# Performance work log

Measured on AMD Instinct MI355X. Metric: run time of the kernel, lower is better.

## Reference

```python
import jax, jax.numpy as jnp
import numpy as np

B, N, IN_CH = 16, 2048, 128
H, C = 4, 64
HC = H * C
E = 524288
NT = B * N
FC0, FC1 = 1024, 512
OMIC = 128
OUT = 2
LN_EPS = 1e-5


def setup_inputs() -> dict:
    key = jax.random.key(0)
    ks = jax.random.split(key, 32)
    s = 0.02
    d = {}
    d['x'] = jax.random.normal(ks[0], (NT, IN_CH), jnp.float32)
    d['edge_index'] = jax.random.randint(ks[1], (2, E), 0, NT, dtype=jnp.int64)
    # GATConv 1: Linear(IN_CH, H*C, bias=False), att_src/att_dst [H,C], bias [H*C]
    d['w1'] = jax.random.normal(ks[2], (IN_CH, HC), jnp.float32) * s
    d['att_src1'] = jax.random.normal(ks[3], (H, C), jnp.float32) * s
    d['att_dst1'] = jax.random.normal(ks[4], (H, C), jnp.float32) * s
    d['bias1'] = jnp.zeros((HC,), jnp.float32)
    d['pool1_w'] = jax.random.normal(ks[5], (HC, 1), jnp.float32) * s
    d['pool1_b'] = jnp.zeros((1,), jnp.float32)
    # GATConv 2: in = H*C
    d['w2'] = jax.random.normal(ks[6], (HC, HC), jnp.float32) * s
    d['att_src2'] = jax.random.normal(ks[7], (H, C), jnp.float32) * s
    d['att_dst2'] = jax.random.normal(ks[8], (H, C), jnp.float32) * s
    d['bias2'] = jnp.zeros((HC,), jnp.float32)
    d['pool2_w'] = jax.random.normal(ks[9], (HC, 1), jnp.float32) * s
    d['pool2_b'] = jnp.zeros((1,), jnp.float32)
    # LayerNorm(num_nodes)
    d['ln_w'] = jnp.ones((N,), jnp.float32)
    d['ln_b'] = jnp.zeros((N,), jnp.float32)
    # FC encoder: Linear(3N, FC0)+ELU, Linear(FC0, FC1)+ELU, Linear(FC1, OMIC)+ELU
    d['enc0_w'] = jax.random.normal(ks[10], (3 * N, FC0), jnp.float32) * s
    d['enc0_b'] = jnp.zeros((FC0,), jnp.float32)
    d['enc1_w'] = jax.random.normal(ks[11], (FC0, FC1), jnp.float32) * s
    d['enc1_b'] = jnp.zeros((FC1,), jnp.float32)
    d['enc2_w'] = jax.random.normal(ks[12], (FC1, OMIC), jnp.float32) * s
    d['enc2_b'] = jnp.zeros((OMIC,), jnp.float32)
    d['last_w'] = jax.random.normal(ks[13], (OMIC, OUT), jnp.float32) * s
    d['last_b'] = jnp.zeros((OUT,), jnp.float32)
    return d


def layer_norm(v, w, b):
    mu = jnp.mean(v, axis=-1, keepdims=True)
    var = jnp.mean((v - mu) ** 2, axis=-1, keepdims=True)
    return (v - mu) * jax.lax.rsqrt(var + LN_EPS) * w + b


def gat_conv(x, src, dst, w, att_src, att_dst, bias):
    # x: [NT, F_in] -> transformed per head [NT, H, C]
    xw = (x @ w).reshape(NT, H, C)
    a_src = jnp.einsum('nhc,hc->nh', xw, att_src)  # [NT, H]
    a_dst = jnp.einsum('nhc,hc->nh', xw, att_dst)
    alpha = jax.nn.leaky_relu(a_src[src] + a_dst[dst], negative_slope=0.2)  # [E', H]
    amax = jax.ops.segment_max(alpha, dst, num_segments=NT)
    ea = jnp.exp(alpha - amax[dst])
    denom = jax.ops.segment_sum(ea, dst, num_segments=NT)
    coef = ea / (denom[dst] + 1e-16)
    msg = xw[src] * coef[:, :, None]  # [E', H, C]
    out = jax.ops.segment_sum(msg, dst, num_segments=NT)
    return out.reshape(NT, HC) + bias


def reference(x, edge_index, w1, att_src1, att_dst1, bias1, pool1_w, pool1_b,
              w2, att_src2, att_dst2, bias2, pool2_w, pool2_b,
              ln_w, ln_b, enc0_w, enc0_b, enc1_w, enc1_b, enc2_w, enc2_b,
              last_w, last_b):
    # add self-loops (GATConv default)
    loops = jnp.arange(NT, dtype=edge_index.dtype)
    src = jnp.concatenate([edge_index[0], loops])
    dst = jnp.concatenate([edge_index[1], loops])
    # layer1 feature: per-node mean, densified to [B, N]
    x0 = layer_norm(jnp.mean(x, axis=-1).reshape(B, N), ln_w, ln_b)
    # GAT layer 1 (dropout is identity in eval)
    h = jax.nn.elu(gat_conv(x, src, dst, w1, att_src1, att_dst1, bias1))
    x1 = layer_norm((h @ pool1_w + pool1_b)[:, 0].reshape(B, N), ln_w, ln_b)
    # GAT layer 2
    h = jax.nn.elu(gat_conv(h, src, dst, w2, att_src2, att_dst2, bias2))
    x2 = layer_norm((h @ pool2_w + pool2_b)[:, 0].reshape(B, N), ln_w, ln_b)
    feat = jnp.concatenate([x0, x1, x2], axis=1)  # [B, 3N]
    e = jax.nn.elu(feat @ enc0_w + enc0_b)
    e = jax.nn.elu(e @ enc1_w + enc1_b)
    e = jax.nn.elu(e @ enc2_w + enc2_b)
    return e @ last_w + last_b  # [B, OUT]
```

## Files before the change

kernel.cpp:

```cpp
#include <hip/hip_runtime.h>
#include <math.h>

#define NTN 32768
#define BB 16
#define NN 2048
#define IN_CH 128
#define HC 256
#define EREAL 524288
#define ETOT (EREAL + NTN)
#define FC0 1024
#define FC1 512
#define OMIC 128
#define OUTD 2
#define CAP 96

#define PREP_BLKS (NTN / 4)
#define DEG_BLKS (EREAL / 256)
#define CASTW_BLKS ((HC * IN_CH + HC * HC) / 256)

typedef __attribute__((ext_vector_type(8))) short bf16x8;
typedef __attribute__((ext_vector_type(4))) float f32x4;

static __device__ __forceinline__ float wave_sum(float v) {
    for (int o = 32; o; o >>= 1) v += __shfl_xor(v, o);
    return v;
}
static __device__ __forceinline__ unsigned short f2bf(float f) {
    unsigned u = __float_as_uint(f);
    unsigned r = (u + 0x7fff + ((u >> 16) & 1)) >> 16;
    return (unsigned short)r;
}
static __device__ __forceinline__ void fma8(uint4 v, float e, float* acc) {
    acc[0] += __uint_as_float(v.x << 16) * e;
    acc[1] += __uint_as_float(v.x & 0xffff0000u) * e;
    acc[2] += __uint_as_float(v.y << 16) * e;
    acc[3] += __uint_as_float(v.y & 0xffff0000u) * e;
    acc[4] += __uint_as_float(v.z << 16) * e;
    acc[5] += __uint_as_float(v.z & 0xffff0000u) * e;
    acc[6] += __uint_as_float(v.w << 16) * e;
    acc[7] += __uint_as_float(v.w & 0xffff0000u) * e;
}

__global__ __launch_bounds__(256) void k_pre(
    const float* __restrict__ x, unsigned short* __restrict__ xb, float* __restrict__ xmean,
    const int* __restrict__ ei, int* __restrict__ deg, int* __restrict__ epos,
    const float* __restrict__ w1, const float* __restrict__ w2,
    unsigned short* __restrict__ w1t, unsigned short* __restrict__ w2t) {
    int b = blockIdx.x, t = threadIdx.x;
    if (b < PREP_BLKS) {
        int wave = t >> 6, lane = t & 63;
        int n = b * 4 + wave;
        float2 v = *(const float2*)(x + (size_t)n * IN_CH + lane * 2);
        ushort2 o;
        o.x = f2bf(v.x); o.y = f2bf(v.y);
        *(ushort2*)(xb + (size_t)n * IN_CH + lane * 2) = o;
        float s = wave_sum(v.x + v.y);
        if (lane == 0) xmean[n] = s * (1.0f / 128.0f);
    } else if (b < PREP_BLKS + DEG_BLKS) {
        int e = (b - PREP_BLKS) * 256 + t;
        int d = ei[EREAL + e];
        epos[e] = atomicAdd(&deg[d], 1);
    } else {
        int idx = (b - PREP_BLKS - DEG_BLKS) * 256 + t;
        if (idx < HC * IN_CH) {
            int n = idx / IN_CH, k = idx % IN_CH;
            w1t[idx] = f2bf(w1[(size_t)k * HC + n]);
        } else {
            int j = idx - HC * IN_CH;
            int n = j / HC, k = j % HC;
            w2t[j] = f2bf(w2[(size_t)k * HC + n]);
        }
    }
}

__global__ __launch_bounds__(1024) void k_scan(const int* __restrict__ deg, int* __restrict__ rowptr,
                                               int* __restrict__ csr) {
    __shared__ int sd[1024];
    int t = threadIdx.x;
    int base = t * 32;
    int loc[32];
    int s = 0;
#pragma unroll
    for (int j = 0; j < 32; j++) { int d = deg[base + j] + 1; loc[j] = d; s += d; }
    sd[t] = s; __syncthreads();
    for (int o = 1; o < 1024; o <<= 1) {
        int v = (t >= o) ? sd[t - o] : 0;
        __syncthreads();
        sd[t] += v;
        __syncthreads();
    }
    int run = sd[t] - s;
#pragma unroll
    for (int j = 0; j < 32; j++) {
        rowptr[base + j] = run;
        csr[run] = base + j;
        run += loc[j];
    }
    if (t == 1023) rowptr[NTN] = run;
}

__global__ void k_fill(const int* __restrict__ ei, const int* __restrict__ epos,
                       const int* __restrict__ rowptr, int* __restrict__ csr) {
    int e = blockIdx.x * 256 + threadIdx.x;
    if (e >= EREAL) return;
    int s = ei[e], d = ei[EREAL + e];
    csr[rowptr[d] + 1 + epos[e]] = s;
}

__global__ __launch_bounds__(256) void k_gemm_mfma(
    const unsigned short* __restrict__ A, const unsigned short* __restrict__ Bt, int K,
    const float* __restrict__ attS, const float* __restrict__ attD,
    unsigned short* __restrict__ Cout, float* __restrict__ aS, float* __restrict__ aD) {
    __shared__ unsigned short As[128][72];
    __shared__ unsigned short Bs[64][72];
    const int t = threadIdx.x;
    const int lane = t & 63, wave = t >> 6;
    const int quad = lane >> 4, l16 = lane & 15;
    const int bx = blockIdx.x, by = blockIdx.y;
    const int arow = t >> 1, acol = (t & 1) * 32;
    const int brow = t >> 2, bcol = (t & 3) * 16;
    const unsigned short* Ag = A + (size_t)(by * 128 + arow) * K + acol;
    const unsigned short* Bg = Bt + (size_t)(bx * 64 + brow) * K + bcol;
    f32x4 acc[2][4] = {};
    for (int k0 = 0; k0 < K; k0 += 64) {
        uint4 a0 = *(const uint4*)(Ag + k0);
        uint4 a1 = *(const uint4*)(Ag + k0 + 8);
        uint4 a2 = *(const uint4*)(Ag + k0 + 16);
        uint4 a3 = *(const uint4*)(Ag + k0 + 24);
        uint4 b0 = *(const uint4*)(Bg + k0);
        uint4 b1 = *(const uint4*)(Bg + k0 + 8);
        __syncthreads();
        *(uint4*)&As[arow][acol +  0] = a0;
        *(uint4*)&As[arow][acol +  8] = a1;
        *(uint4*)&As[arow][acol + 16] = a2;
        *(uint4*)&As[arow][acol + 24] = a3;
        *(uint4*)&Bs[brow][bcol +  0] = b0;
        *(uint4*)&Bs[brow][bcol +  8] = b1;
        __syncthreads();
#pragma unroll
        for (int kc = 0; kc < 64; kc += 32) {
            bf16x8 af[2], bfr[4];
#pragma unroll
            for (int mt = 0; mt < 2; mt++)
                af[mt] = *(const bf16x8*)&As[wave * 32 + mt * 16 + l16][kc + quad * 8];
#pragma unroll
            for (int nt = 0; nt < 4; nt++)
                bfr[nt] = *(const bf16x8*)&Bs[nt * 16 + l16][kc + quad * 8];
#pragma unroll
            for (int mt = 0; mt < 2; mt++)
#pragma unroll
                for (int nt = 0; nt < 4; nt++)
                    acc[mt][nt] = __builtin_amdgcn_mfma_f32_16x16x32_bf16(af[mt], bfr[nt], acc[mt][nt], 0, 0, 0);
        }
    }
    float as_l[4], ad_l[4];
#pragma unroll
    for (int nt = 0; nt < 4; nt++) {
        int gcol = bx * 64 + nt * 16 + l16;
        as_l[nt] = attS[gcol];
        ad_l[nt] = attD[gcol];
    }
#pragma unroll
    for (int mt = 0; mt < 2; mt++) {
#pragma unroll
        for (int reg = 0; reg < 4; reg++) {
            int grow = by * 128 + wave * 32 + mt * 16 + quad * 4 + reg;
            float ps = 0.f, pd = 0.f;
#pragma unroll
            for (int nt = 0; nt < 4; nt++) {
                float v = acc[mt][nt][reg];
                Cout[(size_t)grow * HC + bx * 64 + nt * 16 + l16] = f2bf(v);
                ps += v * as_l[nt];
                pd += v * ad_l[nt];
            }
            for (int o = 8; o; o >>= 1) { ps += __shfl_xor(ps, o); pd += __shfl_xor(pd, o); }
            if (l16 == 0) { aS[grow * 4 + bx] = ps; aD[grow * 4 + bx] = pd; }
        }
    }
}

__global__ __launch_bounds__(256) void k_agg(
    const unsigned short* __restrict__ xw, const float* __restrict__ aS, const float* __restrict__ aD,
    const int* __restrict__ rowptr, const int* __restrict__ csr,
    const float* __restrict__ bias, const float* __restrict__ poolw, const float* __restrict__ poolb,
    unsigned short* __restrict__ hout, float* __restrict__ xpre) {
    __shared__ float ea_s[2][CAP][4];
    __shared__ float part[2][2][256];
    __shared__ float lpart[2][2][4];
    int t = threadIdx.x;
    int wave = t >> 6, lane = t & 63;
    int nd = wave >> 1, half = wave & 1;
    int n = blockIdx.x * 2 + nd;
    int beg = rowptr[n], end = rowptr[n + 1];
    int deg = end - beg;
    int mid = beg + ((deg + 1) >> 1);
    int wbeg = half ? mid : beg;
    int wend = half ? end : mid;
    float4 ad4 = *(const float4*)(aD + n * 4);
    float l0 = 0.f, l1 = 0.f, l2 = 0.f, l3 = 0.f;
    for (int i = wbeg + lane; i < wend; i += 64) {
        int s = csr[i];
        float4 as4 = *(const float4*)(aS + s * 4);
        float a0 = as4.x + ad4.x; a0 = a0 > 0.f ? a0 : 0.2f * a0; float e0 = __expf(a0);
        float a1 = as4.y + ad4.y; a1 = a1 > 0.f ? a1 : 0.2f * a1; float e1 = __expf(a1);
        float a2 = as4.z + ad4.z; a2 = a2 > 0.f ? a2 : 0.2f * a2; float e2 = __expf(a2);
        float a3 = as4.w + ad4.w; a3 = a3 > 0.f ? a3 : 0.2f * a3; float e3 = __expf(a3);
        l0 += e0; l1 += e1; l2 += e2; l3 += e3;
        int j = i - beg;
        if (j < CAP) {
            float4 e4; e4.x = e0; e4.y = e1; e4.z = e2; e4.w = e3;
            *(float4*)&ea_s[nd][j][0] = e4;
        }
    }
    l0 = wave_sum(l0); l1 = wave_sum(l1); l2 = wave_sum(l2); l3 = wave_sum(l3);
    if (lane == 0) {
        lpart[nd][half][0] = l0; lpart[nd][half][1] = l1;
        lpart[nd][half][2] = l2; lpart[nd][half][3] = l3;
    }
    __syncthreads();
    int l31 = lane & 31, hi = lane >> 5;
    int head = l31 >> 3;
    float ilh = 1.0f / (lpart[nd][0][head] + lpart[nd][1][head] + 1e-16f);
    float adh = head == 0 ? ad4.x : head == 1 ? ad4.y : head == 2 ? ad4.z : ad4.w;
    float accA[8] = {}, accB[8] = {};
    const unsigned short* xwc = xw + l31 * 8;
    if (deg <= CAP) {
        int i = wbeg;
        for (; i + 4 <= wend; i += 4) {
            int sA = csr[i + hi];
            int sB = csr[i + 2 + hi];
            float eA = ea_s[nd][i + hi - beg][head];
            float eB = ea_s[nd][i + 2 + hi - beg][head];
            uint4 vA = *(const uint4*)(xwc + (size_t)sA * HC);
            uint4 vB = *(const uint4*)(xwc + (size_t)sB * HC);
            fma8(vA, eA, accA);
            fma8(vB, eB, accB);
        }
        for (; i < wend; i += 2) {
            int idx = i + hi;
            bool ok = idx < wend;
            int sA = csr[ok ? idx : wbeg];
            float eA = ok ? ea_s[nd][idx - beg][head] : 0.f;
            uint4 vA = *(const uint4*)(xwc + (size_t)sA * HC);
            fma8(vA, eA, accA);
        }
    } else {
        for (int i = wbeg; i < wend; i += 2) {
            int idx = i + hi;
            bool ok = idx < wend;
            int sA = csr[ok ? idx : wbeg];
            float a = aS[sA * 4 + head] + adh;
            a = a > 0.f ? a : 0.2f * a;
            float eA = ok ? __expf(a) : 0.f;
            uint4 vA = *(const uint4*)(xwc + (size_t)sA * HC);
            fma8(vA, eA, accA);
        }
    }
    float r8[8];
#pragma unroll
    for (int j = 0; j < 8; j++) {
        float v = accA[j] + accB[j];
        v += __shfl_xor(v, 32);
        r8[j] = v;
    }
    if (hi == 0) {
        float4 q0; q0.x = r8[0]; q0.y = r8[1]; q0.z = r8[2]; q0.w = r8[3];
        float4 q1; q1.x = r8[4]; q1.y = r8[5]; q1.z = r8[6]; q1.w = r8[7];
        *(float4*)&part[nd][half][l31 * 8] = q0;
        *(float4*)&part[nd][half][l31 * 8 + 4] = q1;
    }
    __syncthreads();
    if (half == 0 && hi == 0) {
        float4 p00 = *(const float4*)&part[nd][0][l31 * 8];
        float4 p01 = *(const float4*)&part[nd][0][l31 * 8 + 4];
        float4 p10 = *(const float4*)&part[nd][1][l31 * 8];
        float4 p11 = *(const float4*)&part[nd][1][l31 * 8 + 4];
        float4 b0 = *(const float4*)(bias + l31 * 8);
        float4 b1 = *(const float4*)(bias + l31 * 8 + 4);
        float r[8];
        r[0] = (p00.x + p10.x) * ilh + b0.x;
        r[1] = (p00.y + p10.y) * ilh + b0.y;
        r[2] = (p00.z + p10.z) * ilh + b0.z;
        r[3] = (p00.w + p10.w) * ilh + b0.w;
        r[4] = (p01.x + p11.x) * ilh + b1.x;
        r[5] = (p01.y + p11.y) * ilh + b1.y;
        r[6] = (p01.z + p11.z) * ilh + b1.z;
        r[7] = (p01.w + p11.w) * ilh + b1.w;
#pragma unroll
        for (int j = 0; j < 8; j++) r[j] = r[j] > 0.f ? r[j] : expm1f(r[j]);
        if (hout) {
            uint4 o;
            o.x = (unsigned)f2bf(r[0]) | ((unsigned)f2bf(r[1]) << 16);
            o.y = (unsigned)f2bf(r[2]) | ((unsigned)f2bf(r[3]) << 16);
            o.z = (unsigned)f2bf(r[4]) | ((unsigned)f2bf(r[5]) << 16);
            o.w = (unsigned)f2bf(r[6]) | ((unsigned)f2bf(r[7]) << 16);
            *(uint4*)(hout + (size_t)n * HC + l31 * 8) = o;
        }
        float4 w0 = *(const float4*)(poolw + l31 * 8);
        float4 w1v = *(const float4*)(poolw + l31 * 8 + 4);
        float p = r[0] * w0.x + r[1] * w0.y + r[2] * w0.z + r[3] * w0.w +
                  r[4] * w1v.x + r[5] * w1v.y + r[6] * w1v.z + r[7] * w1v.w;
        for (int o = 16; o; o >>= 1) p += __shfl_xor(p, o);
        if (l31 == 0) xpre[n] = p + poolb[0];
    }
}

__global__ __launch_bounds__(256) void k_ln3(const float* __restrict__ xmean, const float* __restrict__ x1pre,
                                             const float* __restrict__ x2pre, const float* __restrict__ lw,
                                             const float* __restrict__ lb, float* __restrict__ feat) {
    __shared__ float r0[256], r1[256];
    int b = blockIdx.x, t = threadIdx.x;
    int row = b & 15, seg = b >> 4;
    const float* src = (seg == 0 ? xmean : seg == 1 ? x1pre : x2pre) + (size_t)row * NN;
    float* dst = feat + (size_t)row * (3 * NN) + seg * NN;
    float v[8];
    float s = 0.f, s2 = 0.f;
#pragma unroll
    for (int j = 0; j < 8; j++) {
        float x = src[t + j * 256];
        v[j] = x; s += x; s2 += x * x;
    }
    r0[t] = s; r1[t] = s2; __syncthreads();
    for (int o = 128; o; o >>= 1) {
        if (t < o) { r0[t] += r0[t + o]; r1[t] += r1[t + o]; }
        __syncthreads();
    }
    float mu = r0[0] * (1.0f / NN);
    float var = r1[0] * (1.0f / NN) - mu * mu;
    float rs = rsqrtf(var + 1e-5f);
#pragma unroll
    for (int j = 0; j < 8; j++) {
        int idx = t + j * 256;
        dst[idx] = (v[j] - mu) * rs * lw[idx] + lb[idx];
    }
}

template<int KC>
__global__ __launch_bounds__(256) void k_fc_splitk(const float* __restrict__ In, const float* __restrict__ W,
                                                   float* __restrict__ partial, int K, int Nc) {
    __shared__ float in_s[16][KC];
    int t = threadIdx.x;
    int k0 = blockIdx.y * KC;
    for (int idx = t; idx < 16 * KC; idx += 256) {
        int r = idx / KC, kk = idx % KC;
        in_s[r][kk] = In[(size_t)r * K + k0 + kk];
    }
    __syncthreads();
    int col = blockIdx.x * 256 + t;
    if (col < Nc) {
        float acc[16] = {};
#pragma unroll
        for (int kk = 0; kk < KC; kk++) {
            float w = W[(size_t)(k0 + kk) * Nc + col];
#pragma unroll
            for (int r = 0; r < 16; r++) acc[r] += in_s[r][kk] * w;
        }
        float* pp = partial + ((size_t)blockIdx.y * 16) * Nc + col;
#pragma unroll
        for (int r = 0; r < 16; r++) pp[(size_t)r * Nc] = acc[r];
    }
}

template<int KS>
__global__ __launch_bounds__(256) void k_fc_reduce(const float* __restrict__ partial, const float* __restrict__ bias,
                                                   float* __restrict__ Out, int Nc) {
    __shared__ float sm[256];
    int t = threadIdx.x;
    int col = blockIdx.x * 32 + (t & 31);
    int r = blockIdx.y;
    int h = t >> 5;
    float s = 0.f;
#pragma unroll
    for (int i = 0; i < KS / 8; i++)
        s += partial[((size_t)(h + 8 * i) * 16 + r) * Nc + col];
    sm[t] = s;
    __syncthreads();
    if (t < 32) {
        float v = sm[t] + sm[t + 32] + sm[t + 64] + sm[t + 96] +
                  sm[t + 128] + sm[t + 160] + sm[t + 192] + sm[t + 224];
        v += bias[col];
        v = v > 0.f ? v : expm1f(v);
        Out[(size_t)r * Nc + col] = v;
    }
}

__global__ __launch_bounds__(256) void k_last(const float* __restrict__ In, const float* __restrict__ W,
                                              const float* __restrict__ b, float* __restrict__ Out) {
    int t = threadIdx.x;
    int r = t >> 4, c = (t >> 3) & 1, ksub = t & 7;
    float s = 0.f;
#pragma unroll
    for (int k = 0; k < OMIC / 8; k++) s += In[r * OMIC + k * 8 + ksub] * W[(k * 8 + ksub) * OUTD + c];
    for (int o = 1; o < 8; o <<= 1) s += __shfl_xor(s, o);
    if (ksub == 0) Out[r * OUTD + c] = s + b[c];
}

extern "C" void kernel_launch(void* const* d_in, const int* in_sizes, int n_in,
                              void* d_out, int out_size, void* d_ws, size_t ws_size,
                              hipStream_t stream) {
    (void)in_sizes; (void)n_in; (void)out_size; (void)ws_size;
    const float* x        = (const float*)d_in[0];
    const int*   ei       = (const int*)d_in[1];
    const float* w1       = (const float*)d_in[2];
    const float* att_src1 = (const float*)d_in[3];
    const float* att_dst1 = (const float*)d_in[4];
    const float* bias1    = (const float*)d_in[5];
    const float* pool1_w  = (const float*)d_in[6];
    const float* pool1_b  = (const float*)d_in[7];
    const float* w2       = (const float*)d_in[8];
    const float* att_src2 = (const float*)d_in[9];
    const float* att_dst2 = (const float*)d_in[10];
    const float* bias2    = (const float*)d_in[11];
    const float* pool2_w  = (const float*)d_in[12];
    const float* pool2_b  = (const float*)d_in[13];
    const float* ln_w     = (const float*)d_in[14];
    const float* ln_b     = (const float*)d_in[15];
    const float* enc0_w   = (const float*)d_in[16];
    const float* enc0_b   = (const float*)d_in[17];
    const float* enc1_w   = (const float*)d_in[18];
    const float* enc1_b   = (const float*)d_in[19];
    const float* enc2_w   = (const float*)d_in[20];
    const float* enc2_b   = (const float*)d_in[21];
    const float* last_w   = (const float*)d_in[22];
    const float* last_b   = (const float*)d_in[23];
    float* out = (float*)d_out;

    char* p = (char*)d_ws;
    auto alloc = [&](size_t bytes) -> void* {
        void* r = (void*)p;
        p += (bytes + 255) & ~(size_t)255;
        return r;
    };
    unsigned short* xwb  = (unsigned short*)alloc((size_t)NTN * HC * 2);
    unsigned short* hb   = (unsigned short*)alloc((size_t)NTN * HC * 2);
    unsigned short* xb   = (unsigned short*)alloc((size_t)NTN * IN_CH * 2);
    unsigned short* w1t  = (unsigned short*)alloc((size_t)HC * IN_CH * 2);
    unsigned short* w2t  = (unsigned short*)alloc((size_t)HC * HC * 2);
    float* a_src  = (float*)alloc((size_t)NTN * 4 * 4);
    float* a_dst  = (float*)alloc((size_t)NTN * 4 * 4);
    float* xmean  = (float*)alloc((size_t)NTN * 4);
    float* x1pre  = (float*)alloc((size_t)NTN * 4);
    float* x2pre  = (float*)alloc((size_t)NTN * 4);
    float* feat   = (float*)alloc((size_t)BB * 3 * NN * 4);
    float* e0     = (float*)alloc((size_t)BB * FC0 * 4);
    float* e1     = (float*)alloc((size_t)BB * FC1 * 4);
    float* e2     = (float*)alloc((size_t)BB * OMIC * 4);
    float* part0  = (float*)alloc((size_t)96 * 16 * FC0 * 4);
    float* part1  = (float*)alloc((size_t)64 * 16 * FC1 * 4);
    float* part2  = (float*)alloc((size_t)32 * 16 * OMIC * 4);
    int*   deg    = (int*)alloc((size_t)NTN * 4);
    int*   rowptr = (int*)alloc((size_t)(NTN + 1) * 4);
    int*   epos   = (int*)alloc((size_t)EREAL * 4);
    int*   csr    = (int*)alloc((size_t)ETOT * 4);

    hipMemsetAsync(deg, 0, (size_t)NTN * 4, stream);

    k_pre<<<PREP_BLKS + DEG_BLKS + CASTW_BLKS, 256, 0, stream>>>(
        x, xb, xmean, ei, deg, epos, w1, w2, w1t, w2t);
    k_scan<<<1, 1024, 0, stream>>>(deg, rowptr, csr);
    k_fill<<<(EREAL + 255) / 256, 256, 0, stream>>>(ei, epos, rowptr, csr);

    k_gemm_mfma<<<dim3(4, NTN / 128), 256, 0, stream>>>(xb, w1t, IN_CH, att_src1, att_dst1, xwb, a_src, a_dst);
    k_agg<<<NTN / 2, 256, 0, stream>>>(xwb, a_src, a_dst, rowptr, csr, bias1, pool1_w, pool1_b, hb, x1pre);

    k_gemm_mfma<<<dim3(4, NTN / 128), 256, 0, stream>>>(hb, w2t, HC, att_src2, att_dst2, xwb, a_src, a_dst);
    k_agg<<<NTN / 2, 256, 0, stream>>>(xwb, a_src, a_dst, rowptr, csr, bias2, pool2_w, pool2_b, (unsigned short*)nullptr, x2pre);

    k_ln3<<<48, 256, 0, stream>>>(xmean, x1pre, x2pre, ln_w, ln_b, feat);

    k_fc_splitk<64><<<dim3(4, 96), 256, 0, stream>>>(feat, enc0_w, part0, 3 * NN, FC0);
    k_fc_reduce<96><<<dim3(FC0 / 32, 16), 256, 0, stream>>>(part0, enc0_b, e0, FC0);
    k_fc_splitk<16><<<dim3(2, 64), 256, 0, stream>>>(e0, enc1_w, part1, FC0, FC1);
    k_fc_reduce<64><<<dim3(FC1 / 32, 16), 256, 0, stream>>>(part1, enc1_b, e1, FC1);
    k_fc_splitk<16><<<dim3(1, 32), 256, 0, stream>>>(e1, enc2_w, part2, FC1, OMIC);
    k_fc_reduce<32><<<dim3(OMIC / 32, 16), 256, 0, stream>>>(part2, enc2_b, e2, OMIC);
    k_last<<<1, 256, 0, stream>>>(e2, last_w, last_b, out);
}
```

Measured before the change: 354.8 us.

## Fuse CSR fill into first GEMM launch and use packed FMA in aggregation

Removes the separate k_fill launch and instead appends extra blocks to the first k_gemm_mfma grid that scatter edge sources into the CSR, so the fill overlaps with the first GEMM and one launch is saved. The aggregation kernel's bf16 gather-accumulate now uses v_pk_fma_f32 through inline asm, issuing two FMAs per instruction. This adds some branch overhead to the GEMM kernel and ties CSR construction to the first GEMM's schedule.

```diff
diff --git a/kernel.cpp b/kernel.cpp
--- a/kernel.cpp
+++ b/kernel.cpp
@@ -17,9 +17,12 @@
 #define PREP_BLKS (NTN / 4)
 #define DEG_BLKS (EREAL / 256)
 #define CASTW_BLKS ((HC * IN_CH + HC * HC) / 256)
+#define GEMM_YB (NTN / 128)
+#define FILL_YB 512
 
 typedef __attribute__((ext_vector_type(8))) short bf16x8;
 typedef __attribute__((ext_vector_type(4))) float f32x4;
+typedef __attribute__((ext_vector_type(2))) float f32x2;
 
 static __device__ __forceinline__ float wave_sum(float v) {
     for (int o = 32; o; o >>= 1) v += __shfl_xor(v, o);
@@ -30,15 +33,19 @@
     unsigned r = (u + 0x7fff + ((u >> 16) & 1)) >> 16;
     return (unsigned short)r;
 }
-static __device__ __forceinline__ void fma8(uint4 v, float e, float* acc) {
-    acc[0] += __uint_as_float(v.x << 16) * e;
-    acc[1] += __uint_as_float(v.x & 0xffff0000u) * e;
-    acc[2] += __uint_as_float(v.y << 16) * e;
-    acc[3] += __uint_as_float(v.y & 0xffff0000u) * e;
-    acc[4] += __uint_as_float(v.z << 16) * e;
-    acc[5] += __uint_as_float(v.z & 0xffff0000u) * e;
-    acc[6] += __uint_as_float(v.w << 16) * e;
-    acc[7] += __uint_as_float(v.w & 0xffff0000u) * e;
+static __device__ __forceinline__ void pkfma(f32x2& acc, f32x2 ab, f32x2 e2) {
+    asm("v_pk_fma_f32 %0, %1, %2, %0" : "+v"(acc) : "v"(ab), "v"(e2));
+}
+static __device__ __forceinline__ void fma8pk(uint4 v, f32x2 e2, f32x2* acc) {
+    f32x2 p;
+    p.x = __uint_as_float(v.x << 16); p.y = __uint_as_float(v.x & 0xffff0000u);
+    pkfma(acc[0], p, e2);
+    p.x = __uint_as_float(v.y << 16); p.y = __uint_as_float(v.y & 0xffff0000u);
+    pkfma(acc[1], p, e2);
+    p.x = __uint_as_float(v.z << 16); p.y = __uint_as_float(v.z & 0xffff0000u);
+    pkfma(acc[2], p, e2);
+    p.x = __uint_as_float(v.w << 16); p.y = __uint_as_float(v.w & 0xffff0000u);
+    pkfma(acc[3], p, e2);
 }
 
 __global__ __launch_bounds__(256) void k_pre(
@@ -99,24 +106,24 @@
     if (t == 1023) rowptr[NTN] = run;
 }
 
-__global__ void k_fill(const int* __restrict__ ei, const int* __restrict__ epos,
-                       const int* __restrict__ rowptr, int* __restrict__ csr) {
-    int e = blockIdx.x * 256 + threadIdx.x;
-    if (e >= EREAL) return;
-    int s = ei[e], d = ei[EREAL + e];
-    csr[rowptr[d] + 1 + epos[e]] = s;
-}
-
 __global__ __launch_bounds__(256) void k_gemm_mfma(
     const unsigned short* __restrict__ A, const unsigned short* __restrict__ Bt, int K,
     const float* __restrict__ attS, const float* __restrict__ attD,
-    unsigned short* __restrict__ Cout, float* __restrict__ aS, float* __restrict__ aD) {
+    unsigned short* __restrict__ Cout, float* __restrict__ aS, float* __restrict__ aD,
+    const int* __restrict__ ei, const int* __restrict__ epos,
+    const int* __restrict__ rowptr, int* __restrict__ csr) {
     __shared__ unsigned short As[128][72];
     __shared__ unsigned short Bs[64][72];
     const int t = threadIdx.x;
+    const int bx = blockIdx.x, by = blockIdx.y;
+    if (by >= GEMM_YB) {
+        int e = (((by - GEMM_YB) * 4 + bx)) * 256 + t;
+        int s = ei[e], d = ei[EREAL + e];
+        csr[rowptr[d] + 1 + epos[e]] = s;
+        return;
+    }
     const int lane = t & 63, wave = t >> 6;
     const int quad = lane >> 4, l16 = lane & 15;
-    const int bx = blockIdx.x, by = blockIdx.y;
     const int arow = t >> 1, acol = (t & 1) * 32;
     const int brow = t >> 2, bcol = (t & 3) * 16;
     const unsigned short* Ag = A + (size_t)(by * 128 + arow) * K + acol;
@@ -222,7 +229,7 @@
     int head = l31 >> 3;
     float ilh = 1.0f / (lpart[nd][0][head] + lpart[nd][1][head] + 1e-16f);
     float adh = head == 0 ? ad4.x : head == 1 ? ad4.y : head == 2 ? ad4.z : ad4.w;
-    float accA[8] = {}, accB[8] = {};
+    f32x2 accA[4] = {}, accB[4] = {};
     const unsigned short* xwc = xw + l31 * 8;
     if (deg <= CAP) {
         int i = wbeg;
@@ -233,8 +240,10 @@
             float eB = ea_s[nd][i + 2 + hi - beg][head];
             uint4 vA = *(const uint4*)(xwc + (size_t)sA * HC);
             uint4 vB = *(const uint4*)(xwc + (size_t)sB * HC);
-            fma8(vA, eA, accA);
-            fma8(vB, eB, accB);
+            f32x2 eA2; eA2.x = eA; eA2.y = eA;
+            f32x2 eB2; eB2.x = eB; eB2.y = eB;
+            fma8pk(vA, eA2, accA);
+            fma8pk(vB, eB2, accB);
         }
         for (; i < wend; i += 2) {
             int idx = i + hi;
@@ -242,7 +251,8 @@
             int sA = csr[ok ? idx : wbeg];
             float eA = ok ? ea_s[nd][idx - beg][head] : 0.f;
             uint4 vA = *(const uint4*)(xwc + (size_t)sA * HC);
-            fma8(vA, eA, accA);
+            f32x2 eA2; eA2.x = eA; eA2.y = eA;
+            fma8pk(vA, eA2, accA);
         }
     } else {
         for (int i = wbeg; i < wend; i += 2) {
@@ -253,13 +263,14 @@
             a = a > 0.f ? a : 0.2f * a;
             float eA = ok ? __expf(a) : 0.f;
             uint4 vA = *(const uint4*)(xwc + (size_t)sA * HC);
-            fma8(vA, eA, accA);
+            f32x2 eA2; eA2.x = eA; eA2.y = eA;
+            fma8pk(vA, eA2, accA);
         }
     }
     float r8[8];
 #pragma unroll
     for (int j = 0; j < 8; j++) {
-        float v = accA[j] + accB[j];
+        float v = accA[j >> 1][j & 1] + accB[j >> 1][j & 1];
         v += __shfl_xor(v, 32);
         r8[j] = v;
     }
@@ -458,12 +469,13 @@
     k_pre<<<PREP_BLKS + DEG_BLKS + CASTW_BLKS, 256, 0, stream>>>(
         x, xb, xmean, ei, deg, epos, w1, w2, w1t, w2t);
     k_scan<<<1, 1024, 0, stream>>>(deg, rowptr, csr);
-    k_fill<<<(EREAL + 255) / 256, 256, 0, stream>>>(ei, epos, rowptr, csr);
-
-    k_gemm_mfma<<<dim3(4, NTN / 128), 256, 0, stream>>>(xb, w1t, IN_CH, att_src1, att_dst1, xwb, a_src, a_dst);
+
+    k_gemm_mfma<<<dim3(4, GEMM_YB + FILL_YB), 256, 0, stream>>>(
+        xb, w1t, IN_CH, att_src1, att_dst1, xwb, a_src, a_dst, ei, epos, rowptr, csr);
     k_agg<<<NTN / 2, 256, 0, stream>>>(xwb, a_src, a_dst, rowptr, csr, bias1, pool1_w, pool1_b, hb, x1pre);
 
-    k_gemm_mfma<<<dim3(4, NTN / 128), 256, 0, stream>>>(hb, w2t, HC, att_src2, att_dst2, xwb, a_src, a_dst);
+    k_gemm_mfma<<<dim3(4, GEMM_YB), 256, 0, stream>>>(
+        hb, w2t, HC, att_src2, att_dst2, xwb, a_src, a_dst, ei, epos, rowptr, csr);
     k_agg<<<NTN / 2, 256, 0, stream>>>(xwb, a_src, a_dst, rowptr, csr, bias2, pool2_w, pool2_b, (unsigned short*)nullptr, x2pre);
 
     k_ln3<<<48, 256, 0, stream>>>(xmean, x1pre, x2pre, ln_w, ln_b, feat);
```

Measured after the change: 345.9 us. 2.5% less time.
